# Performance work log

Measured on AMD Instinct MI355X. Metric: run time of the kernel, lower is better.

## Reference

```python
import jax, jax.numpy as jnp
import numpy as np

HEADS = 16
DK = 64
THETA = 10000.0


def _rope(x, cos, sin):
    # x: (B, S, H, dk) -> rotate consecutive pairs as complex numbers
    xr = x.reshape(*x.shape[:-1], -1, 2)
    a, b = xr[..., 0], xr[..., 1]
    c = cos[None, :, None, :]  # (1, S, 1, dk//2)
    s = sin[None, :, None, :]
    out = jnp.stack([a * c - b * s, a * s + b * c], axis=-1)
    return out.reshape(x.shape)


def setup_inputs() -> dict:
    key = jax.random.key(0)
    ks = jax.random.split(key, 5)
    B, S, D = 4, 2048, 1024
    x = jax.random.normal(ks[0], (B, S, D), dtype=jnp.float32)
    scale = 1.0 / np.sqrt(D).astype(np.float32)
    Wq = jax.random.normal(ks[1], (D, D), dtype=jnp.float32) * scale
    Wk = jax.random.normal(ks[2], (D, D), dtype=jnp.float32) * scale
    Wv = jax.random.normal(ks[3], (D, D), dtype=jnp.float32) * scale
    Wo = jax.random.normal(ks[4], (D, D), dtype=jnp.float32) * scale
    # freqs_cis = exp(i * t * theta^{-2j/dk}), represented as cos/sin
    t = jnp.arange(S, dtype=jnp.float32)
    inv_freq = 1.0 / (THETA ** (jnp.arange(0, DK, 2, dtype=jnp.float32) / DK))
    ang = t[:, None] * inv_freq[None, :]  # (S, dk//2)
    return {"in_features": x, "freqs_cos": jnp.cos(ang), "freqs_sin": jnp.sin(ang),
            "Wq": Wq, "Wk": Wk, "Wv": Wv, "Wo": Wo}


def reference(in_features, freqs_cos, freqs_sin, Wq, Wk, Wv, Wo):
    B, S, D = in_features.shape
    H = HEADS
    dk = D // H
    # Linear projections (torch Linear: x @ W.T)
    q = (in_features @ Wq.T).reshape(B, S, H, dk)
    k = (in_features @ Wk.T).reshape(B, S, H, dk)
    v = (in_features @ Wv.T).reshape(B, S, H, dk)
    q = _rope(q, freqs_cos, freqs_sin)
    k = _rope(k, freqs_cos, freqs_sin)
    scale = 1.0 / jnp.sqrt(jnp.asarray(dk, dtype=q.dtype))
    scores = jnp.einsum("bqhd,bkhd->bhqk", q, k) * scale
    mask = jnp.tril(jnp.ones((S, S), dtype=bool))
    scores = jnp.where(mask[None, None, :, :], scores, -jnp.inf)
    attn = jax.nn.softmax(scores, axis=-1)
    out = jnp.einsum("bhqk,bkhd->bqhd", attn, v).reshape(B, S, D)
    return out @ Wo.T
```

## Files before the change

### kernel.cpp

```cpp
#include <hip/hip_runtime.h>
#include <hip/hip_bf16.h>

typedef __attribute__((ext_vector_type(8))) __bf16 bf16x8;
typedef __attribute__((ext_vector_type(4))) __bf16 bf16x4;
typedef __attribute__((ext_vector_type(4))) float f32x4;
typedef __attribute__((ext_vector_type(2))) unsigned int u32x2;

static __device__ __forceinline__ f32x4 mfma_bf16(bf16x8 a, bf16x8 b, f32x4 c) {
  return __builtin_amdgcn_mfma_f32_16x16x32_bf16(a, b, c, 0, 0, 0);
}

static __device__ __forceinline__ void gload_lds16(const void* g, void* l) {
  __builtin_amdgcn_global_load_lds(
      (__attribute__((address_space(1))) unsigned int*)g,
      (__attribute__((address_space(3))) unsigned int*)l, 16, 0, 0);
}

static __device__ __forceinline__ unsigned int cvt_pk_bf16(float lo, float hi) {
  unsigned int r;
  asm volatile("v_cvt_pk_bf16_f32 %0, %1, %2" : "=v"(r) : "v"(lo), "v"(hi));
  return r;
}

__global__ void cvt_bf16(const float* __restrict__ in, __bf16* __restrict__ out, int n4) {
  int i = blockIdx.x * blockDim.x + threadIdx.x;
  if (i >= n4) return;
  f32x4 v = ((const f32x4*)in)[i];
  bf16x4 o;
#pragma unroll
  for (int k = 0; k < 4; ++k) o[k] = (__bf16)v[k];
  ((bf16x4*)out)[i] = o;
}

__global__ void cvt_w4(const float* __restrict__ w0, const float* __restrict__ w1,
                       const float* __restrict__ w2, const float* __restrict__ w3,
                       __bf16* __restrict__ o0, __bf16* __restrict__ o1,
                       __bf16* __restrict__ o2, __bf16* __restrict__ o3) {
  const float* in; __bf16* out;
  switch (blockIdx.y) {
    case 0: in = w0; out = o0; break;
    case 1: in = w1; out = o1; break;
    case 2: in = w2; out = o2; break;
    default: in = w3; out = o3; break;
  }
  int i = blockIdx.x * blockDim.x + threadIdx.x;
  f32x4 v = ((const f32x4*)in)[i];
  bf16x4 o;
#pragma unroll
  for (int k = 0; k < 4; ++k) o[k] = (__bf16)v[k];
  ((bf16x4*)out)[i] = o;
}

#define ISSUE_A(kt, slot)                                                   \
  {                                                                         \
    const int k0 = (kt) * 64;                                               \
    __bf16* d = Al + (slot) * 16384 + t * 8;                                \
    gload_lds16(Ag + k0, d);                                                \
    gload_lds16(Ag + (size_t)64 * K + k0, d + 4096);                        \
    gload_lds16(Ag + (size_t)128 * K + k0, d + 8192);                       \
    gload_lds16(Ag + (size_t)192 * K + k0, d + 12288);                      \
  }
#define ISSUE_B(kt, slot)                                                   \
  {                                                                         \
    const int k0 = (kt) * 64;                                               \
    __bf16* d = Bl + (slot) * 8192 + t * 8;                                 \
    gload_lds16(Wg + k0, d);                                                \
    gload_lds16(Wg + (size_t)64 * K + k0, d + 4096);                        \
  }

#define GEMM_PIPELINE                                                       \
  constexpr int K = 1024;                                                   \
  constexpr int NT = K / 64;                                                \
  extern __shared__ __align__(16) __bf16 dynlds[];                          \
  __bf16* Al = dynlds;                                                      \
  __bf16* Bl = dynlds + 49152;                                              \
  const int t = threadIdx.x;                                                \
  const int lane = t & 63, wave = t >> 6;                                   \
  const int g = lane >> 4, ln = lane & 15;                                  \
  const int wm = wave >> 1, wn = wave & 1;                                  \
  f32x4 acc[4][4] = {};                                                     \
  const int srow8 = t >> 3;                                                 \
  const int scole = (((t & 7) ^ ((t >> 3) & 7)) << 3);                      \
  const __bf16* Ag = A + (size_t)(bm * 256 + srow8) * K + scole;            \
  const __bf16* Wg = W + (size_t)(bn * 128 + srow8) * K + scole;            \
  const int axr = ln & 7;                                                   \
  int aoff[4], boff[4];                                                     \
  _Pragma("unroll") for (int i = 0; i < 4; ++i)                             \
    aoff[i] = (wm * 64 + i * 16 + ln) * 64;                                 \
  _Pragma("unroll") for (int j = 0; j < 4; ++j)                             \
    boff[j] = (wn * 64 + j * 16 + ln) * 64;                                 \
  ISSUE_B(0, 0); ISSUE_A(0, 0); ISSUE_A(1, 1);                              \
  asm volatile("s_waitcnt vmcnt(4)" ::: "memory");                          \
  __builtin_amdgcn_s_barrier();                                             \
  int sa = 0;                                                               \
  for (int tt = 0; tt < NT; ++tt) {                                         \
    const __bf16* Ab = Al + sa * 16384;                                     \
    const __bf16* Bb = Bl + (tt & 1) * 8192;                                \
    bf16x8 af[4], bf[4];                                                    \
    _Pragma("unroll") for (int i = 0; i < 4; ++i)                           \
      af[i] = *(const bf16x8*)(Ab + aoff[i] + ((g ^ axr) << 3));            \
    _Pragma("unroll") for (int j = 0; j < 4; ++j)                           \
      bf[j] = *(const bf16x8*)(Bb + boff[j] + ((g ^ axr) << 3));            \
    if (tt + 1 < NT) ISSUE_B(tt + 1, (tt + 1) & 1);                         \
    if (tt + 2 < NT) ISSUE_A(tt + 2, sa == 0 ? 2 : sa - 1);                 \
    __builtin_amdgcn_s_barrier();                                           \
    asm volatile("s_waitcnt lgkmcnt(0)" ::: "memory");                      \
    __builtin_amdgcn_sched_barrier(0);                                      \
    __builtin_amdgcn_s_setprio(1);                                          \
    _Pragma("unroll") for (int i = 0; i < 4; ++i)                           \
      _Pragma("unroll") for (int j = 0; j < 4; ++j)                         \
        acc[i][j] = mfma_bf16(af[i], bf[j], acc[i][j]);                     \
    __builtin_amdgcn_s_setprio(0);                                          \
    __builtin_amdgcn_s_barrier();                                           \
    _Pragma("unroll") for (int i = 0; i < 4; ++i)                           \
      af[i] = *(const bf16x8*)(Ab + aoff[i] + (((4 | g) ^ axr) << 3));      \
    _Pragma("unroll") for (int j = 0; j < 4; ++j)                           \
      bf[j] = *(const bf16x8*)(Bb + boff[j] + (((4 | g) ^ axr) << 3));      \
    if (tt < NT - 2) { asm volatile("s_waitcnt vmcnt(4)" ::: "memory"); }   \
    else             { asm volatile("s_waitcnt vmcnt(0)" ::: "memory"); }   \
    __builtin_amdgcn_s_barrier();                                           \
    asm volatile("s_waitcnt lgkmcnt(0)" ::: "memory");                      \
    __builtin_amdgcn_sched_barrier(0);                                      \
    __builtin_amdgcn_s_setprio(1);                                          \
    _Pragma("unroll") for (int i = 0; i < 4; ++i)                           \
      _Pragma("unroll") for (int j = 0; j < 4; ++j)                         \
        acc[i][j] = mfma_bf16(af[i], bf[j], acc[i][j]);                     \
    __builtin_amdgcn_s_setprio(0);                                          \
    __builtin_amdgcn_s_barrier();                                           \
    sa = (sa == 2) ? 0 : sa + 1;                                            \
  }

__global__ __launch_bounds__(512, 1)
void gemm_qkv(const __bf16* __restrict__ A,
              const __bf16* __restrict__ Wqp, const __bf16* __restrict__ Wkp,
              const __bf16* __restrict__ Wvp,
              __bf16* __restrict__ Qo, __bf16* __restrict__ Ko,
              __bf16* __restrict__ Vo,
              const float* __restrict__ fcos, const float* __restrict__ fsin) {
  const int lin = blockIdx.x + blockIdx.y * 24;
  const int bm = (lin & 7) + 8 * ((lin >> 3) / 24);
  const int bn3 = (lin >> 3) % 24;
  const int mode = bn3 >> 3, bn = bn3 & 7;
  const __bf16* W = (mode == 0) ? Wqp : (mode == 1) ? Wkp : Wvp;

  GEMM_PIPELINE

#pragma unroll
  for (int i = 0; i < 4; ++i) {
    const int mbase = bm * 256 + wm * 64 + i * 16 + g * 4;
#pragma unroll
    for (int j = 0; j < 4; ++j) {
      const int col = bn * 128 + wn * 64 + j * 16 + ln;
      if (mode < 2) {
        const int fi = (col & 63) >> 1;
        const bool odd = (col & 1) != 0;
        __bf16* O = (mode == 0) ? Qo : Ko;
        const float sc = (mode == 0) ? 0.1803368802f : 1.0f;
#pragma unroll
        for (int r = 0; r < 4; ++r) {
          const int row = mbase + r;
          const int tok = row & 2047;
          const float cs = fcos[tok * 32 + fi];
          const float sn = fsin[tok * 32 + fi];
          const float own = acc[i][j][r];
          const float oth = __shfl_xor(own, 1);
          O[(size_t)row * 1024 + col] =
              (__bf16)((own * cs + (odd ? oth * sn : -oth * sn)) * sc);
        }
      } else {
        const int bb = mbase >> 11;
        const int tok = mbase & 2047;
        bf16x4 pk;
#pragma unroll
        for (int r = 0; r < 4; ++r) pk[r] = (__bf16)acc[i][j][r];
        *(bf16x4*)(Vo + ((size_t)(bb * 1024 + col)) * 2048 + tok) = pk;
      }
    }
  }
}

__global__ __launch_bounds__(512, 1)
void gemm_out(const __bf16* __restrict__ A, const __bf16* __restrict__ W,
              float* __restrict__ outp) {
  const int lin = blockIdx.x + blockIdx.y * 8;
  const int bm = (lin & 7) + 8 * ((lin >> 3) & 3);
  const int bn = lin >> 5;

  GEMM_PIPELINE

#pragma unroll
  for (int i = 0; i < 4; ++i) {
    const int mbase = bm * 256 + wm * 64 + i * 16 + g * 4;
#pragma unroll
    for (int j = 0; j < 4; ++j) {
      const int col = bn * 128 + wn * 64 + j * 16 + ln;
#pragma unroll
      for (int r = 0; r < 4; ++r)
        outp[(size_t)(mbase + r) * 1024 + col] = acc[i][j][r];
    }
  }
}

static __device__ __forceinline__ void sm_pack_pv(
    f32x4* sa, float& m, float& l, f32x4* o,
    unsigned int* Pw, const __bf16* Vb, const int g, const int ln) {
  const float a0 = fmaxf(fmaxf(sa[0][0], sa[0][1]), sa[0][2]);
  const float a1 = fmaxf(fmaxf(sa[0][3], sa[1][0]), sa[1][1]);
  const float a2 = fmaxf(fmaxf(sa[1][2], sa[1][3]), sa[2][0]);
  const float a3 = fmaxf(fmaxf(sa[2][1], sa[2][2]), sa[2][3]);
  const float a4 = fmaxf(fmaxf(sa[3][0], sa[3][1]), sa[3][2]);
  float pm = fmaxf(fmaxf(fmaxf(a0, a1), a2), fmaxf(fmaxf(a3, a4), sa[3][3]));

  if (__any(pm > m + 8.f)) {
    pm = fmaxf(pm, __shfl_xor(pm, 16));
    pm = fmaxf(pm, __shfl_xor(pm, 32));
    const float mn = fmaxf(m, pm);
    const float alpha = exp2f(m - mn);
    m = mn;
    l *= alpha;
#pragma unroll
    for (int c2 = 0; c2 < 4; ++c2)
#pragma unroll
      for (int r = 0; r < 4; ++r) o[c2][r] *= alpha;
  }

  float p[4][4];
#pragma unroll
  for (int c = 0; c < 4; ++c)
#pragma unroll
    for (int r = 0; r < 4; ++r) p[c][r] = exp2f(sa[c][r] - m);

  float ts[8];
#pragma unroll
  for (int i = 0; i < 8; ++i) ts[i] = p[i >> 2][i & 3] + p[2 + (i >> 2)][i & 3];
#pragma unroll
  for (int st = 4; st >= 1; st >>= 1)
#pragma unroll
    for (int i = 0; i < st; ++i) ts[i] += ts[i + st];
  float rs = ts[0];
  rs += __shfl_xor(rs, 16);
  rs += __shfl_xor(rs, 32);
  l += rs;

  unsigned int* Pr = Pw + ln * 36;
#pragma unroll
  for (int c = 0; c < 4; ++c) {
    u32x2 w;
    w[0] = cvt_pk_bf16(p[c][0], p[c][1]);
    w[1] = cvt_pk_bf16(p[c][2], p[c][3]);
    *(u32x2*)(Pr + 8 * c + 2 * g) = w;
  }

  __builtin_amdgcn_s_setprio(1);
#pragma unroll
  for (int sh = 0; sh < 2; ++sh) {
    bf16x8 pb = *(const bf16x8*)((const __bf16*)Pw + ln * 72 + sh * 32 + g * 8);
#pragma unroll
    for (int c2 = 0; c2 < 4; ++c2) {
      bf16x8 vf = *(const bf16x8*)(Vb + sh * 2048 + (c2 * 16 + ln) * 32 + g * 8);
      o[c2] = mfma_bf16(vf, pb, o[c2]);
    }
  }
  __builtin_amdgcn_s_setprio(0);
}

__global__ __launch_bounds__(512, 4)
void attn_fwd(const __bf16* __restrict__ Q, const __bf16* __restrict__ Kk,
              const __bf16* __restrict__ Vt, __bf16* __restrict__ U) {
  constexpr int S = 2048;
  __shared__ __align__(16) __bf16 Klds[2][2 * 64 * 32];
  __shared__ __align__(16) __bf16 Vlds[2][2 * 64 * 32];
  __shared__ __align__(16) unsigned int Plds[2][8][16 * 36];

  const int t = threadIdx.x;
  const int lane = t & 63, wave = t >> 6;
  const int g = lane >> 4, ln = lane & 15;
  const int lin = blockIdx.x + blockIdx.y * 8;
  const int bh = (lin & 7) * 8 + ((lin >> 3) & 7);
  const int qt = lin >> 6;
  const int b = bh >> 4, h = bh & 15;
  const int q0s[2] = {qt * 128, (15 - qt) * 128};
  const int nts[2] = {2 * qt + 2, 32 - 2 * qt};

  bf16x8 qf[2][2];
#pragma unroll
  for (int s2 = 0; s2 < 2; ++s2) {
    const __bf16* Qb = Q + ((size_t)(b * S + q0s[s2] + wave * 16 + ln)) * 1024 + h * 64;
    qf[s2][0] = *(const bf16x8*)(Qb + g * 8);
    qf[s2][1] = *(const bf16x8*)(Qb + 32 + g * 8);
  }

  f32x4 o[2][4] = {};
  float mrow[2], lrow[2];
#pragma unroll
  for (int s2 = 0; s2 < 2; ++s2) { mrow[s2] = -3.0e38f; lrow[s2] = 0.f; }

  const int half = t >> 8;
  const int srow = (t >> 2) & 63;
  const int scol = (t & 3) * 8;
  const __bf16* Kg = Kk + ((size_t)(b * S + srow)) * 1024 + h * 64 + half * 32 + scol;
  const __bf16* Vg = Vt + ((size_t)(b * 1024 + h * 64 + srow)) * 2048 + half * 32 + scol;
  const int nt = nts[1];

  gload_lds16(Kg, (__bf16*)Klds[0] + t * 8);
  gload_lds16(Vg, (__bf16*)Vlds[0] + t * 8);
  __syncthreads();

  for (int kt = 0; kt < nt; ++kt) {
    const int cur = kt & 1;
    if (kt + 1 < nt) {
      const size_t kv1 = (size_t)(kt + 1) * 64;
      gload_lds16(Kg + kv1 * 1024, (__bf16*)Klds[cur ^ 1] + t * 8);
      gload_lds16(Vg + kv1, (__bf16*)Vlds[cur ^ 1] + t * 8);
    }
    const int kv0 = kt * 64;

    if (kt < nts[0]) {
      f32x4 sa0[4] = {}, sa1[4] = {};
      __builtin_amdgcn_s_setprio(1);
#pragma unroll
      for (int s = 0; s < 2; ++s) {
#pragma unroll
        for (int c = 0; c < 4; ++c) {
          bf16x8 kf = *(const bf16x8*)(Klds[cur] + s * 2048 + (c * 16 + ln) * 32 + g * 8);
          sa0[c] = mfma_bf16(kf, qf[0][s], sa0[c]);
          sa1[c] = mfma_bf16(kf, qf[1][s], sa1[c]);
        }
      }
      __builtin_amdgcn_s_setprio(0);

      const int rfbase0 = q0s[0] + wave * 16;
      const int rq0 = rfbase0 + ln;
      if (kv0 + 63 > rfbase0) {
#pragma unroll
        for (int c = 0; c < 4; ++c)
#pragma unroll
          for (int r = 0; r < 4; ++r)
            if (kv0 + c * 16 + g * 4 + r > rq0) sa0[c][r] = -1e30f;
      }

      sm_pack_pv(sa0, mrow[0], lrow[0], o[0], Plds[0][wave], Vlds[cur], g, ln);
      sm_pack_pv(sa1, mrow[1], lrow[1], o[1], Plds[1][wave], Vlds[cur], g, ln);
    } else {
      f32x4 sa1[4] = {};
      __builtin_amdgcn_s_setprio(1);
#pragma unroll
      for (int s = 0; s < 2; ++s) {
#pragma unroll
        for (int c = 0; c < 4; ++c) {
          bf16x8 kf = *(const bf16x8*)(Klds[cur] + s * 2048 + (c * 16 + ln) * 32 + g * 8);
          sa1[c] = mfma_bf16(kf, qf[1][s], sa1[c]);
        }
      }
      __builtin_amdgcn_s_setprio(0);

      const int rfbase1 = q0s[1] + wave * 16;
      const int rq1 = rfbase1 + ln;
      if (kv0 + 63 > rfbase1) {
#pragma unroll
        for (int c = 0; c < 4; ++c)
#pragma unroll
          for (int r = 0; r < 4; ++r)
            if (kv0 + c * 16 + g * 4 + r > rq1) sa1[c][r] = -1e30f;
      }

      sm_pack_pv(sa1, mrow[1], lrow[1], o[1], Plds[1][wave], Vlds[cur], g, ln);
    }
    __syncthreads();
  }

#pragma unroll
  for (int s2 = 0; s2 < 2; ++s2) {
    const float rl = 1.0f / lrow[s2];
    __bf16* Ub = U + ((size_t)(b * S + q0s[s2] + wave * 16 + ln)) * 1024 + h * 64;
#pragma unroll
    for (int c2 = 0; c2 < 4; ++c2) {
      bf16x4 pk4;
#pragma unroll
      for (int r = 0; r < 4; ++r) pk4[r] = (__bf16)(o[s2][c2][r] * rl);
      *(bf16x4*)(Ub + 16 * c2 + 4 * g) = pk4;
    }
  }
}

extern "C" void kernel_launch(void* const* d_in, const int* in_sizes, int n_in,
                              void* d_out, int out_size, void* d_ws, size_t ws_size,
                              hipStream_t stream) {
  const float* x    = (const float*)d_in[0];
  const float* fcos = (const float*)d_in[1];
  const float* fsin = (const float*)d_in[2];
  const float* Wq   = (const float*)d_in[3];
  const float* Wk   = (const float*)d_in[4];
  const float* Wv   = (const float*)d_in[5];
  const float* Wo   = (const float*)d_in[6];

  char* ws = (char*)d_ws;
  __bf16* xb  = (__bf16*)(ws);
  __bf16* Wqb = (__bf16*)(ws + (16u << 20));
  __bf16* Wkb = (__bf16*)(ws + (18u << 20));
  __bf16* Wvb = (__bf16*)(ws + (20u << 20));
  __bf16* Wob = (__bf16*)(ws + (22u << 20));
  __bf16* Qb  = (__bf16*)(ws + (24u << 20));
  __bf16* Kb  = (__bf16*)(ws + (40u << 20));
  __bf16* Vtb = (__bf16*)(ws + (56u << 20));
  __bf16* Ub  = xb;

  cvt_bf16<<<8192, 256, 0, stream>>>(x, xb, 8192 * 1024 / 4);
  cvt_w4<<<dim3(1024, 4), 256, 0, stream>>>(Wq, Wk, Wv, Wo, Wqb, Wkb, Wvb, Wob);

  const size_t lds = 131072;
  gemm_qkv<<<dim3(24, 32), 512, lds, stream>>>(xb, Wqb, Wkb, Wvb, Qb, Kb, Vtb,
                                               fcos, fsin);
  attn_fwd<<<dim3(8, 64), 512, 0, stream>>>(Qb, Kb, Vtb, Ub);
  gemm_out<<<dim3(8, 32), 512, lds, stream>>>(Ub, Wob, (float*)d_out);
}
```

Measured before the change: 187.2 us.

## Split paired causal q-tiles into separate attention blocks, heaviest first

The attention kernel no longer pairs a light and a heavy 128-row query tile in one block for load balancing. Each block now handles a single query tile, so the grid doubles to 1024 blocks, and blocks are ordered so the longest causal tiles launch first. The per-block register and LDS footprint roughly halves, and launch bounds are raised to allow more resident blocks. The trade-off is that each loaded K/V tile is reused by only one query tile instead of two, so K/V global traffic roughly doubles, and scheduling now relies on the hardware to balance uneven block lengths.

New measurement: 184.3 us. No clear change (-1.5%).

```diff
diff --git a/kernel.cpp b/kernel.cpp
--- a/kernel.cpp
+++ b/kernel.cpp
@@ -264,43 +264,36 @@
   __builtin_amdgcn_s_setprio(0);
 }
 
-__global__ __launch_bounds__(512, 4)
+__global__ __launch_bounds__(512, 6)
 void attn_fwd(const __bf16* __restrict__ Q, const __bf16* __restrict__ Kk,
               const __bf16* __restrict__ Vt, __bf16* __restrict__ U) {
   constexpr int S = 2048;
   __shared__ __align__(16) __bf16 Klds[2][2 * 64 * 32];
   __shared__ __align__(16) __bf16 Vlds[2][2 * 64 * 32];
-  __shared__ __align__(16) unsigned int Plds[2][8][16 * 36];
+  __shared__ __align__(16) unsigned int Plds[8][16 * 36];
 
   const int t = threadIdx.x;
   const int lane = t & 63, wave = t >> 6;
   const int g = lane >> 4, ln = lane & 15;
-  const int lin = blockIdx.x + blockIdx.y * 8;
+  const int lin = blockIdx.x + blockIdx.y * 16;
   const int bh = (lin & 7) * 8 + ((lin >> 3) & 7);
-  const int qt = lin >> 6;
+  const int qt = 15 - (lin >> 6);
   const int b = bh >> 4, h = bh & 15;
-  const int q0s[2] = {qt * 128, (15 - qt) * 128};
-  const int nts[2] = {2 * qt + 2, 32 - 2 * qt};
-
-  bf16x8 qf[2][2];
-#pragma unroll
-  for (int s2 = 0; s2 < 2; ++s2) {
-    const __bf16* Qb = Q + ((size_t)(b * S + q0s[s2] + wave * 16 + ln)) * 1024 + h * 64;
-    qf[s2][0] = *(const bf16x8*)(Qb + g * 8);
-    qf[s2][1] = *(const bf16x8*)(Qb + 32 + g * 8);
-  }
-
-  f32x4 o[2][4] = {};
-  float mrow[2], lrow[2];
-#pragma unroll
-  for (int s2 = 0; s2 < 2; ++s2) { mrow[s2] = -3.0e38f; lrow[s2] = 0.f; }
+  const int q0 = qt * 128;
+  const int nt = 2 * qt + 2;
+
+  const __bf16* Qb = Q + ((size_t)(b * S + q0 + wave * 16 + ln)) * 1024 + h * 64;
+  bf16x8 qf0 = *(const bf16x8*)(Qb + g * 8);
+  bf16x8 qf1 = *(const bf16x8*)(Qb + 32 + g * 8);
+
+  f32x4 o[4] = {};
+  float mrow = -3.0e38f, lrow = 0.f;
 
   const int half = t >> 8;
   const int srow = (t >> 2) & 63;
   const int scol = (t & 3) * 8;
   const __bf16* Kg = Kk + ((size_t)(b * S + srow)) * 1024 + h * 64 + half * 32 + scol;
   const __bf16* Vg = Vt + ((size_t)(b * 1024 + h * 64 + srow)) * 2048 + half * 32 + scol;
-  const int nt = nts[1];
 
   gload_lds16(Kg, (__bf16*)Klds[0] + t * 8);
   gload_lds16(Vg, (__bf16*)Vlds[0] + t * 8);
@@ -315,71 +308,41 @@
     }
     const int kv0 = kt * 64;
 
-    if (kt < nts[0]) {
-      f32x4 sa0[4] = {}, sa1[4] = {};
-      __builtin_amdgcn_s_setprio(1);
-#pragma unroll
-      for (int s = 0; s < 2; ++s) {
-#pragma unroll
-        for (int c = 0; c < 4; ++c) {
-          bf16x8 kf = *(const bf16x8*)(Klds[cur] + s * 2048 + (c * 16 + ln) * 32 + g * 8);
-          sa0[c] = mfma_bf16(kf, qf[0][s], sa0[c]);
-          sa1[c] = mfma_bf16(kf, qf[1][s], sa1[c]);
-        }
+    f32x4 sa[4] = {};
+    __builtin_amdgcn_s_setprio(1);
+#pragma unroll
+    for (int s = 0; s < 2; ++s) {
+      const bf16x8 qf = s ? qf1 : qf0;
+#pragma unroll
+      for (int c = 0; c < 4; ++c) {
+        bf16x8 kf = *(const bf16x8*)(Klds[cur] + s * 2048 + (c * 16 + ln) * 32 + g * 8);
+        sa[c] = mfma_bf16(kf, qf, sa[c]);
       }
-      __builtin_amdgcn_s_setprio(0);
-
-      const int rfbase0 = q0s[0] + wave * 16;
-      const int rq0 = rfbase0 + ln;
-      if (kv0 + 63 > rfbase0) {
-#pragma unroll
-        for (int c = 0; c < 4; ++c)
-#pragma unroll
-          for (int r = 0; r < 4; ++r)
-            if (kv0 + c * 16 + g * 4 + r > rq0) sa0[c][r] = -1e30f;
-      }
-
-      sm_pack_pv(sa0, mrow[0], lrow[0], o[0], Plds[0][wave], Vlds[cur], g, ln);
-      sm_pack_pv(sa1, mrow[1], lrow[1], o[1], Plds[1][wave], Vlds[cur], g, ln);
-    } else {
-      f32x4 sa1[4] = {};
-      __builtin_amdgcn_s_setprio(1);
-#pragma unroll
-      for (int s = 0; s < 2; ++s) {
-#pragma unroll
-        for (int c = 0; c < 4; ++c) {
-          bf16x8 kf = *(const bf16x8*)(Klds[cur] + s * 2048 + (c * 16 + ln) * 32 + g * 8);
-          sa1[c] = mfma_bf16(kf, qf[1][s], sa1[c]);
-        }
-      }
-      __builtin_amdgcn_s_setprio(0);
-
-      const int rfbase1 = q0s[1] + wave * 16;
-      const int rq1 = rfbase1 + ln;
-      if (kv0 + 63 > rfbase1) {
-#pragma unroll
-        for (int c = 0; c < 4; ++c)
-#pragma unroll
-          for (int r = 0; r < 4; ++r)
-            if (kv0 + c * 16 + g * 4 + r > rq1) sa1[c][r] = -1e30f;
-      }
-
-      sm_pack_pv(sa1, mrow[1], lrow[1], o[1], Plds[1][wave], Vlds[cur], g, ln);
-    }
+    }
+    __builtin_amdgcn_s_setprio(0);
+
+    const int rfbase = q0 + wave * 16;
+    const int rq = rfbase + ln;
+    if (kv0 + 63 > rfbase) {
+#pragma unroll
+      for (int c = 0; c < 4; ++c)
+#pragma unroll
+        for (int r = 0; r < 4; ++r)
+          if (kv0 + c * 16 + g * 4 + r > rq) sa[c][r] = -1e30f;
+    }
+
+    sm_pack_pv(sa, mrow, lrow, o, Plds[wave], Vlds[cur], g, ln);
     __syncthreads();
   }
 
-#pragma unroll
-  for (int s2 = 0; s2 < 2; ++s2) {
-    const float rl = 1.0f / lrow[s2];
-    __bf16* Ub = U + ((size_t)(b * S + q0s[s2] + wave * 16 + ln)) * 1024 + h * 64;
-#pragma unroll
-    for (int c2 = 0; c2 < 4; ++c2) {
-      bf16x4 pk4;
-#pragma unroll
-      for (int r = 0; r < 4; ++r) pk4[r] = (__bf16)(o[s2][c2][r] * rl);
-      *(bf16x4*)(Ub + 16 * c2 + 4 * g) = pk4;
-    }
+  const float rl = 1.0f / lrow;
+  __bf16* Ub = U + ((size_t)(b * S + q0 + wave * 16 + ln)) * 1024 + h * 64;
+#pragma unroll
+  for (int c2 = 0; c2 < 4; ++c2) {
+    bf16x4 pk4;
+#pragma unroll
+    for (int r = 0; r < 4; ++r) pk4[r] = (__bf16)(o[c2][r] * rl);
+    *(bf16x4*)(Ub + 16 * c2 + 4 * g) = pk4;
   }
 }
 
@@ -411,6 +374,6 @@
   const size_t lds = 131072;
   gemm_qkv<<<dim3(24, 32), 512, lds, stream>>>(xb, Wqb, Wkb, Wvb, Qb, Kb, Vtb,
                                                fcos, fsin);
-  attn_fwd<<<dim3(8, 64), 512, 0, stream>>>(Qb, Kb, Vtb, Ub);
+  attn_fwd<<<dim3(16, 64), 512, 0, stream>>>(Qb, Kb, Vtb, Ub);
   gemm_out<<<dim3(8, 32), 512, lds, stream>>>(Ub, Wob, (float*)d_out);
 }
```
